# Optimization experiments

Measured on AMD Instinct MI355X. Metric: run time of the kernel, lower is better.

Reference implementation:

```python
import jax, jax.numpy as jnp
import numpy as np

N, D_IN, D_LAT, D_FEAT, K = 12000, 64, 16, 64, 16


def setup_inputs() -> dict:
    key = jax.random.key(0)
    ks = jax.random.split(key, 7)
    s_in = 1.0 / np.sqrt(D_IN)
    s_cat = 1.0 / np.sqrt(2 * D_FEAT)
    return {
        "x": jax.random.normal(ks[0], (N, D_IN), dtype=jnp.float32),
        "W_feat": jax.random.uniform(ks[1], (D_IN, D_FEAT), jnp.float32, -s_in, s_in),
        "b_feat": jax.random.uniform(ks[2], (D_FEAT,), jnp.float32, -s_in, s_in),
        "W_lat": jax.random.uniform(ks[3], (D_IN, D_LAT), jnp.float32, -s_in, s_in),
        "b_lat": jax.random.uniform(ks[4], (D_LAT,), jnp.float32, -s_in, s_in),
        "W_out": jax.random.uniform(ks[5], (2 * D_FEAT, D_FEAT), jnp.float32, -s_cat, s_cat),
        "b_out": jax.random.uniform(ks[6], (D_FEAT,), jnp.float32, -s_cat, s_cat),
    }


def reference(x, W_feat, b_feat, W_lat, b_lat, W_out, b_out):
    # dense encoders
    feats = jnp.tanh(x @ W_feat + b_feat)      # [N, F] learned features
    coords = jnp.tanh(x @ W_lat + b_lat)       # [N, S] latent coordinates
    n = coords.shape[0]
    # full pairwise squared euclidean distances (as the module's cdist)
    sq = jnp.sum(coords * coords, axis=1)
    d2 = sq[:, None] + sq[None, :] - 2.0 * (coords @ coords.T)   # [N, N]
    d2 = jnp.maximum(d2, 0.0)
    # knn_graph: k nearest neighbors, excluding self (loop=False)
    d2_masked = jnp.where(jnp.eye(n, dtype=bool), jnp.inf, d2)
    neg_d2, idx = jax.lax.top_k(-d2_masked, K)                   # idx: [N, K] neighbor (source) ids
    edge_d2 = -neg_d2                                            # squared dist to each neighbor
    # gaussian kernel on euclidean distance: w = exp(-d^2)
    w = jnp.exp(-edge_d2)                                        # [N, K]
    # message = w * x_j, aggr='add': out_i = sum_k w_ik * feats[idx_ik]
    agg = jnp.einsum('nk,nkf->nf', w, feats[idx])                # [N, F]
    # cat self features with aggregated messages, final dense
    out = jnp.concatenate([feats, agg], axis=1) @ W_out + b_out  # [N, F]
    return out
```

## Files before the change

kernel.cpp:

```cpp
#include <hip/hip_runtime.h>
#include <math.h>

typedef unsigned long long u64;
typedef _Float16 f16x8 __attribute__((ext_vector_type(8)));
typedef float f32x16 __attribute__((ext_vector_type(16)));

#define N_PTS 12000
#define KNN 16
#define QB 16
#define NWAVES 8
#define NGROUPS32 (N_PTS / 32)
#define TAU_PTS 2048
#define TAU_GROUPS32 (TAU_PTS / 32)
#define CAP 384
#define MARGIN 0.08f
#define EVICT_KEY ((u64)0x7F400000u << 32)

__global__ __launch_bounds__(256) void encoder_kernel(
    const float* __restrict__ x, const float* __restrict__ Wf, const float* __restrict__ bf,
    const float* __restrict__ Wl, const float* __restrict__ bl,
    float* __restrict__ feats, float* __restrict__ coords, _Float16* __restrict__ coords_h,
    float* __restrict__ sq)
{
  const int wave = threadIdx.x >> 6;
  const int lane = threadIdx.x & 63;
  const int i = blockIdx.x * 4 + wave;
  if (i >= N_PTS) return;
  float xv = x[i * 64 + lane];
  float accf = bf[lane];
  float accc = bl[lane & 15];
  #pragma unroll
  for (int k = 0; k < 64; ++k) {
    float xk = __shfl(xv, k);
    accf = fmaf(xk, Wf[k * 64 + lane], accf);
    accc = fmaf(xk, Wl[k * 16 + (lane & 15)], accc);
  }
  feats[i * 64 + lane] = tanhf(accf);
  float c = tanhf(accc);
  float cc = (lane < 16) ? c * c : 0.0f;
  cc += __shfl_xor(cc, 1);
  cc += __shfl_xor(cc, 2);
  cc += __shfl_xor(cc, 4);
  cc += __shfl_xor(cc, 8);
  if (lane < 16) {
    coords[i * 16 + lane] = c;
    coords_h[i * 16 + lane] = (_Float16)c;
  }
  if (lane == 0) sq[i] = cc;
}

__device__ __forceinline__ void ins6(u64 key, u64* k6, u64& kmax) {
  const u64 om = (key < kmax) ? kmax : ~0ull;
  #pragma unroll
  for (int t = 0; t < 6; ++t)
    k6[t] = (k6[t] == om) ? key : k6[t];
  u64 a = k6[0] > k6[1] ? k6[0] : k6[1];
  u64 b = k6[2] > k6[3] ? k6[2] : k6[3];
  u64 c = k6[4] > k6[5] ? k6[4] : k6[5];
  a = a > b ? a : b;
  kmax = a > c ? a : c;
}

__device__ __forceinline__ void ins8(u64 key, u64* k8, u64& kmax) {
  const u64 om = (key < kmax) ? kmax : ~0ull;
  #pragma unroll
  for (int t = 0; t < 8; ++t)
    k8[t] = (k8[t] == om) ? key : k8[t];
  u64 a = k8[0] > k8[1] ? k8[0] : k8[1];
  u64 b = k8[2] > k8[3] ? k8[2] : k8[3];
  u64 c = k8[4] > k8[5] ? k8[4] : k8[5];
  u64 d = k8[6] > k8[7] ? k8[6] : k8[7];
  a = a > b ? a : b;
  c = c > d ? c : d;
  kmax = a > c ? a : c;
}

__device__ __forceinline__ u64 shflx_u64(u64 v, int off) {
  int lo = __shfl_xor((int)(unsigned)v, off);
  int hi = __shfl_xor((int)(unsigned)(v >> 32), off);
  return ((u64)(unsigned)hi << 32) | (unsigned)lo;
}

__device__ __forceinline__ u64 minbfly(u64 m) {
  #pragma unroll
  for (int off = 32; off >= 1; off >>= 1) {
    u64 o = shflx_u64(m, off);
    m = (o < m) ? o : m;
  }
  return m;
}

#define CAS6(i, j) { const u64 a_ = k6[i], b_ = k6[j]; const bool sw_ = a_ > b_; \
                     k6[i] = sw_ ? b_ : a_; k6[j] = sw_ ? a_ : b_; }

__global__ __launch_bounds__(512) void knn_agg_kernel(
    const float* __restrict__ coords, const _Float16* __restrict__ coords_h,
    const float* __restrict__ sq, const float* __restrict__ feats,
    const float* __restrict__ Wo, const float* __restrict__ bo,
    float* __restrict__ out, int* __restrict__ flags)
{
  __shared__ unsigned short sbuf[QB][CAP];
  __shared__ int scnt[QB];
  __shared__ unsigned colminS[QB][64];
  __shared__ float taugS[QB];
  __shared__ __align__(16) float featS[QB][64];
  __shared__ __align__(16) float aggS[QB][64];

  const int tid = threadIdx.x;
  const int lane = tid & 63;
  const int wave = tid >> 6;
  const int qbase = blockIdx.x * QB;
  const int mcol = lane & 31;
  const int half = lane >> 5;

  if (tid < QB) scnt[tid] = 0;
  #pragma unroll
  for (int t = tid; t < QB * 64; t += 512)
    ((unsigned*)colminS)[t] = 0x7F800000u;

  f16x8 afrag = {0, 0, 0, 0, 0, 0, 0, 0};
  if (mcol < QB) {
    const uint4 u = *(const uint4*)((const char*)coords_h + (qbase + mcol) * 32 + half * 16);
    afrag = __builtin_bit_cast(f16x8, u);
  }
  float sqi8[8], nhsqi8[8];
  #pragma unroll
  for (int blk = 0; blk < 2; ++blk) {
    const float4 v = *(const float4*)&sq[qbase + blk * 8 + 4 * half];
    sqi8[blk * 4 + 0] = v.x; sqi8[blk * 4 + 1] = v.y;
    sqi8[blk * 4 + 2] = v.z; sqi8[blk * 4 + 3] = v.w;
  }
  #pragma unroll
  for (int r = 0; r < 8; ++r) nhsqi8[r] = -0.5f * sqi8[r];

  f32x16 acc;
  #pragma unroll
  for (int t = 0; t < 16; ++t) acc[t] = 0.0f;

  __syncthreads();

  const int g_self = qbase >> 5;
  float lmax8[8] = {-INFINITY, -INFINITY, -INFINITY, -INFINITY,
                    -INFINITY, -INFINITY, -INFINITY, -INFINITY};
  for (int g = wave; g < TAU_GROUPS32; g += NWAVES) {
    const int j0 = g * 32;
    const uint4 u = *(const uint4*)((const char*)coords_h + (j0 + mcol) * 32 + half * 16);
    const f16x8 bfrag = __builtin_bit_cast(f16x8, u);
    const float sqj = sq[j0 + mcol];
    #pragma unroll
    for (int r = 0; r < 8; ++r) acc[r] = fmaf(-0.5f, sqj, nhsqi8[r]);
    acc = __builtin_amdgcn_mfma_f32_32x32x16_f16(afrag, bfrag, acc, 0, 0, 0);
    if (g == g_self) {
      #pragma unroll
      for (int r = 0; r < 8; ++r) {
        const int row = (r >> 2) * 8 + 4 * half + (r & 3);
        if (j0 + mcol == qbase + row) acc[r] = -INFINITY;
      }
    }
    #pragma unroll
    for (int r = 0; r < 8; ++r) lmax8[r] = fmaxf(lmax8[r], acc[r]);
  }
  {
    const int cell = mcol * 2 + (wave >> 2);
    #pragma unroll
    for (int r = 0; r < 8; ++r) {
      const int row = (r >> 2) * 8 + 4 * half + (r & 3);
      atomicMin(&colminS[row][cell], __float_as_uint(fmaxf(-2.0f * lmax8[r], 0.0f)));
    }
  }
  __syncthreads();

  #pragma unroll
  for (int s = 0; s < 2; ++s) {
    const int q = wave * 2 + s;
    float v = __uint_as_float(colminS[q][lane]);
    #pragma unroll
    for (int k = 2; k <= 64; k <<= 1) {
      #pragma unroll
      for (int st = k >> 1; st >= 1; st >>= 1) {
        const float o = __shfl_xor(v, st);
        const bool keepMin = (((lane & st) == 0) == ((lane & k) == 0));
        const float mn = fminf(v, o), mx = fmaxf(v, o);
        v = keepMin ? mn : mx;
      }
    }
    const float tq = __shfl(v, 15) + MARGIN;
    if (lane == 0) taugS[q] = tq;
  }
  __syncthreads();

  float nht8[8];
  #pragma unroll
  for (int r = 0; r < 8; ++r)
    nht8[r] = -0.5f * taugS[(r >> 2) * 8 + 4 * half + (r & 3)];

  #pragma unroll 2
  for (int g = wave; g < NGROUPS32; g += NWAVES) {
    const int j0 = g * 32;
    const uint4 u = *(const uint4*)((const char*)coords_h + (j0 + mcol) * 32 + half * 16);
    const f16x8 bfrag = __builtin_bit_cast(f16x8, u);
    const float sqj = sq[j0 + mcol];
    #pragma unroll
    for (int r = 0; r < 8; ++r) acc[r] = fmaf(-0.5f, sqj, nhsqi8[r]);
    acc = __builtin_amdgcn_mfma_f32_32x32x16_f16(afrag, bfrag, acc, 0, 0, 0);
    #pragma unroll
    for (int r = 0; r < 8; ++r) {
      const bool pass = acc[r] >= nht8[r];
      if (__any(pass)) {
        if (pass) {
          const int row = (r >> 2) * 8 + 4 * half + (r & 3);
          const int p = atomicAdd(&scnt[row], 1);
          if (p < CAP) sbuf[row][p] = (unsigned short)(j0 + mcol);
        }
      }
    }
  }
  __syncthreads();

  #pragma unroll
  for (int s = 0; s < 2; ++s) {
    const int lq = wave * 2 + s;
    const int qg = qbase + lq;
    const int cq = scnt[lq];
    const int nread = (cq < CAP) ? cq : CAP;
    const int nit = (nread + 63) >> 6;

    float ci[16];
    {
      const float4* cp = (const float4*)(coords + qg * 16);
      *(float4*)&ci[0] = cp[0]; *(float4*)&ci[4] = cp[1];
      *(float4*)&ci[8] = cp[2]; *(float4*)&ci[12] = cp[3];
    }
    const float sqiq = sq[qg];

    u64 k6[6];
    #pragma unroll
    for (int t = 0; t < 6; ++t) k6[t] = ((u64)(0x7F000000u + t) << 32);
    u64 kmax6 = ((u64)0x7F000005u << 32);

    for (int t = 0; t < nit; ++t) {
      const int idx = t * 64 + lane;
      u64 key = ~0ull;
      if (idx < nread) {
        const int jj = sbuf[lq][idx];
        if (jj != qg) {
          const float4* cp = (const float4*)(coords + jj * 16);
          float cj[16];
          *(float4*)&cj[0]  = cp[0]; *(float4*)&cj[4]  = cp[1];
          *(float4*)&cj[8]  = cp[2]; *(float4*)&cj[12] = cp[3];
          float dot = 0.0f;
          #pragma unroll
          for (int d = 0; d < 16; ++d) dot = fmaf(ci[d], cj[d], dot);
          const float d2 = fmaxf(fmaf(-2.0f, dot, sqiq + sq[jj]), 0.0f);
          key = ((u64)__float_as_uint(d2) << 32) | (unsigned)jj;
        }
      }
      ins6(key, k6, kmax6);
    }

    CAS6(0,5) CAS6(1,3) CAS6(2,4)
    CAS6(1,2) CAS6(3,4)
    CAS6(0,3) CAS6(2,5)
    CAS6(0,1) CAS6(2,3) CAS6(4,5)
    CAS6(1,2) CAS6(3,4)

    float dmin = __uint_as_float((unsigned)(k6[0] >> 32));
    int jmin = (int)(unsigned)(k6[0] & 0xFFFFFFFFull);

    float dv[16]; int jv[16];
    #pragma unroll
    for (int r = 0; r < KNN; ++r) {
      float m = dmin;
      #pragma unroll
      for (int off = 32; off >= 1; off >>= 1)
        m = fminf(m, __shfl_xor(m, off));
      const u64 bal = __ballot(dmin == m);
      const int owner = __ffsll((unsigned long long)bal) - 1;
      jv[r] = __builtin_amdgcn_readlane(jmin, owner);
      dv[r] = __uint_as_float(__builtin_amdgcn_readfirstlane(__float_as_uint(m)));
      const bool me = (lane == owner);
      k6[0] = me ? k6[1] : k6[0];
      k6[1] = me ? k6[2] : k6[1];
      k6[2] = me ? k6[3] : k6[2];
      k6[3] = me ? k6[4] : k6[3];
      k6[4] = me ? k6[5] : k6[4];
      k6[5] = me ? EVICT_KEY : k6[5];
      dmin = __uint_as_float((unsigned)(k6[0] >> 32));
      jmin = (int)(unsigned)(k6[0] & 0xFFFFFFFFull);
    }

    float aggv = 0.0f;
    #pragma unroll
    for (int r = 0; r < KNN; ++r)
      aggv = fmaf(__expf(-dv[r]), feats[jv[r] * 64 + lane], aggv);

    aggS[lq][lane] = aggv;
    featS[lq][lane] = feats[qg * 64 + lane];
    if (lane == 0) flags[qg] = (cq > CAP);
  }

  __syncthreads();
  const int row = tid >> 5;
  const int c2 = (tid & 31) * 2;
  float acc0 = bo[c2], acc1 = bo[c2 + 1];
  #pragma unroll
  for (int f0 = 0; f0 < 64; f0 += 4) {
    const float4 fv = *(const float4*)&featS[row][f0];
    const float4 av = *(const float4*)&aggS[row][f0];
    #pragma unroll
    for (int u = 0; u < 4; ++u) {
      const float fvu = (u == 0) ? fv.x : (u == 1) ? fv.y : (u == 2) ? fv.z : fv.w;
      const float avu = (u == 0) ? av.x : (u == 1) ? av.y : (u == 2) ? av.z : av.w;
      const float2 w0 = *(const float2*)&Wo[(f0 + u) * 64 + c2];
      const float2 w1 = *(const float2*)&Wo[(64 + f0 + u) * 64 + c2];
      acc0 = fmaf(fvu, w0.x, acc0); acc0 = fmaf(avu, w1.x, acc0);
      acc1 = fmaf(fvu, w0.y, acc1); acc1 = fmaf(avu, w1.y, acc1);
    }
  }
  const int orow = qbase + row;
  *(float2*)&out[orow * 64 + c2] = make_float2(acc0, acc1);
}

__global__ __launch_bounds__(256) void knn_fixup_kernel(
    const float* __restrict__ coords, const float* __restrict__ sq,
    const float* __restrict__ feats, const int* __restrict__ flags,
    const float* __restrict__ Wo, const float* __restrict__ bo,
    float* __restrict__ out)
{
  const int wave = threadIdx.x >> 6;
  const int lane = threadIdx.x & 63;
  const int i = blockIdx.x * 4 + wave;
  if (i >= N_PTS) return;
  if (!flags[i]) return;
  float ci[16];
  #pragma unroll
  for (int d = 0; d < 16; ++d) ci[d] = coords[i * 16 + d];
  const float sqi = sq[i];

  u64 k8a[8], k8b[8], kmaxA, kmaxB;
  #pragma unroll
  for (int t = 0; t < 8; ++t) {
    k8a[t] = ((u64)(0x7F000000u + t) << 32);
    k8b[t] = ((u64)(0x7F000000u + t) << 32);
  }
  kmaxA = ((u64)0x7F000007u << 32);
  kmaxB = ((u64)0x7F000007u << 32);

  const int niter = (N_PTS + 63) / 64;
  for (int t = 0; t < niter; ++t) {
    const int j = t * 64 + lane;
    float4 c0 = make_float4(0,0,0,0), c1 = c0, c2 = c0, c3 = c0;
    float sqj = 0.0f;
    if (j < N_PTS) {
      const float4* cp = (const float4*)(coords + j * 16);
      c0 = cp[0]; c1 = cp[1]; c2 = cp[2]; c3 = cp[3];
      sqj = sq[j];
    }
    float dot = ci[0]*c0.x + ci[1]*c0.y + ci[2]*c0.z + ci[3]*c0.w
              + ci[4]*c1.x + ci[5]*c1.y + ci[6]*c1.z + ci[7]*c1.w
              + ci[8]*c2.x + ci[9]*c2.y + ci[10]*c2.z + ci[11]*c2.w
              + ci[12]*c3.x + ci[13]*c3.y + ci[14]*c3.z + ci[15]*c3.w;
    float d2 = fmaxf(fmaf(-2.0f, dot, sqi + sqj), 0.0f);
    const unsigned hi = (j == i || j >= N_PTS) ? 0xFFFFFFFFu : __float_as_uint(d2);
    const u64 key = ((u64)hi << 32) | (unsigned)j;
    if (t & 1) ins8(key, k8a, kmaxA);
    else       ins8(key, k8b, kmaxB);
  }

  u64 tab[16];
  #pragma unroll
  for (int t = 0; t < 8; ++t) { tab[t] = k8a[t]; tab[8 + t] = k8b[t]; }
  u64 lmin = tab[0];
  #pragma unroll
  for (int t = 1; t < 16; ++t) lmin = (tab[t] < lmin) ? tab[t] : lmin;

  float aggv = 0.0f;
  u64 T16 = 0;
  for (int r = 0; r < KNN; ++r) {
    const u64 m = minbfly(lmin);
    if (lmin == m) {
      #pragma unroll
      for (int t = 0; t < 16; ++t) tab[t] = (tab[t] == m) ? ~0ull : tab[t];
      lmin = tab[0];
      #pragma unroll
      for (int t = 1; t < 16; ++t) lmin = (tab[t] < lmin) ? tab[t] : lmin;
    }
    const unsigned hi = (unsigned)(m >> 32);
    const bool ok = hi < 0x7F000000u;
    const float w = ok ? expf(-__uint_as_float(hi)) : 0.0f;
    const int jj = ok ? (int)(unsigned)(m & 0xFFFFFFFFull) : 0;
    aggv = fmaf(w, feats[jj * 64 + lane], aggv);
    T16 = m;
  }

  if (__any((kmaxA < T16) || (kmaxB < T16))) {
    aggv = 0.0f;
    u64 prev = 0;
    for (int r = 0; r < KNN; ++r) {
      u64 best = ~0ull;
      for (int j = lane; j < N_PTS; j += 64) {
        float dot = 0.0f;
        #pragma unroll
        for (int d = 0; d < 16; ++d) dot = fmaf(ci[d], coords[j * 16 + d], dot);
        const float d2 = fmaxf(fmaf(-2.0f, dot, sqi + sq[j]), 0.0f);
        const unsigned hi = (j == i) ? 0xFFFFFFFFu : __float_as_uint(d2);
        const u64 key = ((u64)hi << 32) | (unsigned)j;
        const bool cand = (r == 0) || (key > prev);
        if (cand && key < best) best = key;
      }
      const u64 m = minbfly(best);
      prev = m;
      const unsigned hi = (unsigned)(m >> 32);
      const bool ok = hi < 0x7F000000u;
      const float w = ok ? expf(-__uint_as_float(hi)) : 0.0f;
      const int jj = ok ? (int)(unsigned)(m & 0xFFFFFFFFull) : 0;
      aggv = fmaf(w, feats[jj * 64 + lane], aggv);
    }
  }

  const float fl = feats[i * 64 + lane];
  float acc = bo[lane];
  #pragma unroll
  for (int f = 0; f < 64; ++f) {
    acc = fmaf(__shfl(fl, f),   Wo[f * 64 + lane],        acc);
    acc = fmaf(__shfl(aggv, f), Wo[(64 + f) * 64 + lane], acc);
  }
  out[i * 64 + lane] = acc;
}

extern "C" void kernel_launch(void* const* d_in, const int* in_sizes, int n_in,
                              void* d_out, int out_size, void* d_ws, size_t ws_size,
                              hipStream_t stream) {
  const float* x  = (const float*)d_in[0];
  const float* Wf = (const float*)d_in[1];
  const float* bf = (const float*)d_in[2];
  const float* Wl = (const float*)d_in[3];
  const float* bl = (const float*)d_in[4];
  const float* Wo = (const float*)d_in[5];
  const float* bo = (const float*)d_in[6];
  float* out = (float*)d_out;

  char* ws = (char*)d_ws;
  float*     feats    = (float*)(ws);
  float*     coords   = (float*)(ws + 3072000);
  float*     sqv      = (float*)(ws + 3840000);
  _Float16*  coords_h = (_Float16*)(ws + 3888000);
  int*       flags    = (int*)(ws + 4272000);

  encoder_kernel<<<3000, 256, 0, stream>>>(x, Wf, bf, Wl, bl, feats, coords, coords_h, sqv);
  knn_agg_kernel<<<N_PTS / QB, 512, 0, stream>>>(coords, coords_h, sqv, feats, Wo, bo, out, flags);
  knn_fixup_kernel<<<3000, 256, 0, stream>>>(coords, sqv, feats, flags, Wo, bo, out);
}
```

Baseline: 174.3 us.

## Prefetch coordinate tiles, split top-k merge across half-waves, double tau sample

Adds a three-deep register prefetch of coordinate fragments and squared norms in both the threshold-estimation and candidate-filtering MFMA loops, and removes the wave-wide any() guard. It also doubles the sample used to estimate the per-query distance threshold, splits the encoder's dot products into two accumulators, and sets occupancy launch bounds. The final 16-way selection now merges both queries' candidate lists at once, each half-wave working over 32 lanes and writing keys to shared memory. These aim to hide global load latency and shorten the serial selection, at the cost of more registers and twice the threshold-sampling work.

```diff
diff --git a/kernel.cpp b/kernel.cpp
--- a/kernel.cpp
+++ b/kernel.cpp
@@ -10,7 +10,7 @@
 #define QB 16
 #define NWAVES 8
 #define NGROUPS32 (N_PTS / 32)
-#define TAU_PTS 2048
+#define TAU_PTS 4096
 #define TAU_GROUPS32 (TAU_PTS / 32)
 #define CAP 384
 #define MARGIN 0.08f
@@ -27,16 +27,19 @@
   const int i = blockIdx.x * 4 + wave;
   if (i >= N_PTS) return;
   float xv = x[i * 64 + lane];
-  float accf = bf[lane];
-  float accc = bl[lane & 15];
-  #pragma unroll
-  for (int k = 0; k < 64; ++k) {
-    float xk = __shfl(xv, k);
-    accf = fmaf(xk, Wf[k * 64 + lane], accf);
-    accc = fmaf(xk, Wl[k * 16 + (lane & 15)], accc);
-  }
-  feats[i * 64 + lane] = tanhf(accf);
-  float c = tanhf(accc);
+  float accf0 = bf[lane], accf1 = 0.0f;
+  float accc0 = bl[lane & 15], accc1 = 0.0f;
+  #pragma unroll
+  for (int k = 0; k < 64; k += 2) {
+    const float xk0 = __shfl(xv, k);
+    const float xk1 = __shfl(xv, k + 1);
+    accf0 = fmaf(xk0, Wf[k * 64 + lane], accf0);
+    accf1 = fmaf(xk1, Wf[(k + 1) * 64 + lane], accf1);
+    accc0 = fmaf(xk0, Wl[k * 16 + (lane & 15)], accc0);
+    accc1 = fmaf(xk1, Wl[(k + 1) * 16 + (lane & 15)], accc1);
+  }
+  feats[i * 64 + lane] = tanhf(accf0 + accf1);
+  float c = tanhf(accc0 + accc1);
   float cc = (lane < 16) ? c * c : 0.0f;
   cc += __shfl_xor(cc, 1);
   cc += __shfl_xor(cc, 2);
@@ -93,7 +96,11 @@
 #define CAS6(i, j) { const u64 a_ = k6[i], b_ = k6[j]; const bool sw_ = a_ > b_; \
                      k6[i] = sw_ ? b_ : a_; k6[j] = sw_ ? a_ : b_; }
 
-__global__ __launch_bounds__(512) void knn_agg_kernel(
+#define LOADG(g, uu, ss) { const int jl_ = (g) * 32 + mcol; \
+  uu = *(const uint4*)((const char*)coords_h + (size_t)jl_ * 32 + half * 16); \
+  ss = sq[jl_]; }
+
+__global__ __launch_bounds__(512, 6) void knn_agg_kernel(
     const float* __restrict__ coords, const _Float16* __restrict__ coords_h,
     const float* __restrict__ sq, const float* __restrict__ feats,
     const float* __restrict__ Wo, const float* __restrict__ bo,
@@ -103,6 +110,7 @@
   __shared__ int scnt[QB];
   __shared__ unsigned colminS[QB][64];
   __shared__ float taugS[QB];
+  __shared__ u64 keyS[QB][KNN];
   __shared__ __align__(16) float featS[QB][64];
   __shared__ __align__(16) float aggS[QB][64];
 
@@ -123,15 +131,13 @@
     const uint4 u = *(const uint4*)((const char*)coords_h + (qbase + mcol) * 32 + half * 16);
     afrag = __builtin_bit_cast(f16x8, u);
   }
-  float sqi8[8], nhsqi8[8];
+  float nhsqi8[8];
   #pragma unroll
   for (int blk = 0; blk < 2; ++blk) {
     const float4 v = *(const float4*)&sq[qbase + blk * 8 + 4 * half];
-    sqi8[blk * 4 + 0] = v.x; sqi8[blk * 4 + 1] = v.y;
-    sqi8[blk * 4 + 2] = v.z; sqi8[blk * 4 + 3] = v.w;
-  }
-  #pragma unroll
-  for (int r = 0; r < 8; ++r) nhsqi8[r] = -0.5f * sqi8[r];
+    nhsqi8[blk * 4 + 0] = -0.5f * v.x; nhsqi8[blk * 4 + 1] = -0.5f * v.y;
+    nhsqi8[blk * 4 + 2] = -0.5f * v.z; nhsqi8[blk * 4 + 3] = -0.5f * v.w;
+  }
 
   f32x16 acc;
   #pragma unroll
@@ -142,23 +148,33 @@
   const int g_self = qbase >> 5;
   float lmax8[8] = {-INFINITY, -INFINITY, -INFINITY, -INFINITY,
                     -INFINITY, -INFINITY, -INFINITY, -INFINITY};
-  for (int g = wave; g < TAU_GROUPS32; g += NWAVES) {
-    const int j0 = g * 32;
-    const uint4 u = *(const uint4*)((const char*)coords_h + (j0 + mcol) * 32 + half * 16);
-    const f16x8 bfrag = __builtin_bit_cast(f16x8, u);
-    const float sqj = sq[j0 + mcol];
-    #pragma unroll
-    for (int r = 0; r < 8; ++r) acc[r] = fmaf(-0.5f, sqj, nhsqi8[r]);
-    acc = __builtin_amdgcn_mfma_f32_32x32x16_f16(afrag, bfrag, acc, 0, 0, 0);
-    if (g == g_self) {
-      #pragma unroll
-      for (int r = 0; r < 8; ++r) {
-        const int row = (r >> 2) * 8 + 4 * half + (r & 3);
-        if (j0 + mcol == qbase + row) acc[r] = -INFINITY;
+  {
+    uint4 pu0, pu1, pu2; float ps0, ps1, ps2;
+    LOADG(wave,                pu0, ps0);
+    LOADG(wave + NWAVES,       pu1, ps1);
+    LOADG(wave + 2 * NWAVES,   pu2, ps2);
+    for (int k = 0; k < 16; ++k) {
+      const int g = wave + k * NWAVES;
+      const uint4 cu = pu0; const float cs = ps0;
+      pu0 = pu1; ps0 = ps1; pu1 = pu2; ps1 = ps2;
+      const int kn = k + 3;
+      const int gs = (kn < 16) ? (wave + kn * NWAVES) : wave;
+      LOADG(gs, pu2, ps2);
+
+      const f16x8 bfrag = __builtin_bit_cast(f16x8, cu);
+      #pragma unroll
+      for (int r = 0; r < 8; ++r) acc[r] = fmaf(-0.5f, cs, nhsqi8[r]);
+      acc = __builtin_amdgcn_mfma_f32_32x32x16_f16(afrag, bfrag, acc, 0, 0, 0);
+      if (g == g_self) {
+        #pragma unroll
+        for (int r = 0; r < 8; ++r) {
+          const int row = (r >> 2) * 8 + 4 * half + (r & 3);
+          if (g * 32 + mcol == qbase + row) acc[r] = -INFINITY;
+        }
       }
-    }
-    #pragma unroll
-    for (int r = 0; r < 8; ++r) lmax8[r] = fmaxf(lmax8[r], acc[r]);
+      #pragma unroll
+      for (int r = 0; r < 8; ++r) lmax8[r] = fmaxf(lmax8[r], acc[r]);
+    }
   }
   {
     const int cell = mcol * 2 + (wave >> 2);
@@ -194,20 +210,26 @@
   for (int r = 0; r < 8; ++r)
     nht8[r] = -0.5f * taugS[(r >> 2) * 8 + 4 * half + (r & 3)];
 
-  #pragma unroll 2
-  for (int g = wave; g < NGROUPS32; g += NWAVES) {
-    const int j0 = g * 32;
-    const uint4 u = *(const uint4*)((const char*)coords_h + (j0 + mcol) * 32 + half * 16);
-    const f16x8 bfrag = __builtin_bit_cast(f16x8, u);
-    const float sqj = sq[j0 + mcol];
-    #pragma unroll
-    for (int r = 0; r < 8; ++r) acc[r] = fmaf(-0.5f, sqj, nhsqi8[r]);
-    acc = __builtin_amdgcn_mfma_f32_32x32x16_f16(afrag, bfrag, acc, 0, 0, 0);
-    #pragma unroll
-    for (int r = 0; r < 8; ++r) {
-      const bool pass = acc[r] >= nht8[r];
-      if (__any(pass)) {
-        if (pass) {
+  {
+    uint4 pu0, pu1, pu2; float ps0, ps1, ps2;
+    LOADG(wave,                pu0, ps0);
+    LOADG(wave + NWAVES,       pu1, ps1);
+    LOADG(wave + 2 * NWAVES,   pu2, ps2);
+    for (int g = wave; g < NGROUPS32; g += NWAVES) {
+      const uint4 cu = pu0; const float cs = ps0;
+      pu0 = pu1; ps0 = ps1; pu1 = pu2; ps1 = ps2;
+      const int gn = g + 3 * NWAVES;
+      const int gs = (gn < NGROUPS32) ? gn : wave;
+      LOADG(gs, pu2, ps2);
+
+      const f16x8 bfrag = __builtin_bit_cast(f16x8, cu);
+      #pragma unroll
+      for (int r = 0; r < 8; ++r) acc[r] = fmaf(-0.5f, cs, nhsqi8[r]);
+      acc = __builtin_amdgcn_mfma_f32_32x32x16_f16(afrag, bfrag, acc, 0, 0, 0);
+      const int j0 = g * 32;
+      #pragma unroll
+      for (int r = 0; r < 8; ++r) {
+        if (acc[r] >= nht8[r]) {
           const int row = (r >> 2) * 8 + 4 * half + (r & 3);
           const int p = atomicAdd(&scnt[row], 1);
           if (p < CAP) sbuf[row][p] = (unsigned short)(j0 + mcol);
@@ -216,6 +238,9 @@
     }
   }
   __syncthreads();
+
+  const int h = lane >> 5;
+  u64 Al[6], Bl[6];
 
   #pragma unroll
   for (int s = 0; s < 2; ++s) {
@@ -245,12 +270,21 @@
         const int jj = sbuf[lq][idx];
         if (jj != qg) {
           const float4* cp = (const float4*)(coords + jj * 16);
-          float cj[16];
-          *(float4*)&cj[0]  = cp[0]; *(float4*)&cj[4]  = cp[1];
-          *(float4*)&cj[8]  = cp[2]; *(float4*)&cj[12] = cp[3];
           float dot = 0.0f;
-          #pragma unroll
-          for (int d = 0; d < 16; ++d) dot = fmaf(ci[d], cj[d], dot);
+          {
+            const float4 c0 = cp[0], c1 = cp[1];
+            dot = fmaf(ci[0], c0.x, dot); dot = fmaf(ci[1], c0.y, dot);
+            dot = fmaf(ci[2], c0.z, dot); dot = fmaf(ci[3], c0.w, dot);
+            dot = fmaf(ci[4], c1.x, dot); dot = fmaf(ci[5], c1.y, dot);
+            dot = fmaf(ci[6], c1.z, dot); dot = fmaf(ci[7], c1.w, dot);
+          }
+          {
+            const float4 c2 = cp[2], c3 = cp[3];
+            dot = fmaf(ci[8],  c2.x, dot); dot = fmaf(ci[9],  c2.y, dot);
+            dot = fmaf(ci[10], c2.z, dot); dot = fmaf(ci[11], c2.w, dot);
+            dot = fmaf(ci[12], c3.x, dot); dot = fmaf(ci[13], c3.y, dot);
+            dot = fmaf(ci[14], c3.z, dot); dot = fmaf(ci[15], c3.w, dot);
+          }
           const float d2 = fmaxf(fmaf(-2.0f, dot, sqiq + sq[jj]), 0.0f);
           key = ((u64)__float_as_uint(d2) << 32) | (unsigned)jj;
         }
@@ -264,39 +298,52 @@
     CAS6(0,1) CAS6(2,3) CAS6(4,5)
     CAS6(1,2) CAS6(3,4)
 
-    float dmin = __uint_as_float((unsigned)(k6[0] >> 32));
-    int jmin = (int)(unsigned)(k6[0] & 0xFFFFFFFFull);
-
-    float dv[16]; int jv[16];
+    #pragma unroll
+    for (int t = 0; t < 6; ++t) {
+      const u64 p = shflx_u64(k6[t], 32);
+      if (h == s) { Al[t] = k6[t]; Bl[t] = p; }
+    }
+    if (lane == 0) flags[qg] = (cq > CAP);
+  }
+
+  {
+    u64 myhead = (Al[0] < Bl[0]) ? Al[0] : Bl[0];
     #pragma unroll
     for (int r = 0; r < KNN; ++r) {
-      float m = dmin;
-      #pragma unroll
-      for (int off = 32; off >= 1; off >>= 1)
-        m = fminf(m, __shfl_xor(m, off));
-      const u64 bal = __ballot(dmin == m);
-      const int owner = __ffsll((unsigned long long)bal) - 1;
-      jv[r] = __builtin_amdgcn_readlane(jmin, owner);
-      dv[r] = __uint_as_float(__builtin_amdgcn_readfirstlane(__float_as_uint(m)));
-      const bool me = (lane == owner);
-      k6[0] = me ? k6[1] : k6[0];
-      k6[1] = me ? k6[2] : k6[1];
-      k6[2] = me ? k6[3] : k6[2];
-      k6[3] = me ? k6[4] : k6[3];
-      k6[4] = me ? k6[5] : k6[4];
-      k6[5] = me ? EVICT_KEY : k6[5];
-      dmin = __uint_as_float((unsigned)(k6[0] >> 32));
-      jmin = (int)(unsigned)(k6[0] & 0xFFFFFFFFull);
-    }
-
+      u64 m = myhead;
+      #pragma unroll
+      for (int off = 16; off >= 1; off >>= 1) {
+        const u64 o = shflx_u64(m, off);
+        m = (o < m) ? o : m;
+      }
+      if ((lane & 31) == 0) keyS[wave * 2 + h][r] = m;
+      const bool me = (myhead == m);
+      const bool fa = me && (Al[0] == m);
+      const bool fb = me && !fa;
+      Al[0] = fa ? Al[1] : Al[0]; Al[1] = fa ? Al[2] : Al[1];
+      Al[2] = fa ? Al[3] : Al[2]; Al[3] = fa ? Al[4] : Al[3];
+      Al[4] = fa ? Al[5] : Al[4]; Al[5] = fa ? EVICT_KEY : Al[5];
+      Bl[0] = fb ? Bl[1] : Bl[0]; Bl[1] = fb ? Bl[2] : Bl[1];
+      Bl[2] = fb ? Bl[3] : Bl[2]; Bl[3] = fb ? Bl[4] : Bl[3];
+      Bl[4] = fb ? Bl[5] : Bl[4]; Bl[5] = fb ? EVICT_KEY : Bl[5];
+      myhead = (Al[0] < Bl[0]) ? Al[0] : Bl[0];
+    }
+  }
+
+  #pragma unroll
+  for (int s = 0; s < 2; ++s) {
+    const int lq = wave * 2 + s;
+    const int qg = qbase + lq;
     float aggv = 0.0f;
     #pragma unroll
-    for (int r = 0; r < KNN; ++r)
-      aggv = fmaf(__expf(-dv[r]), feats[jv[r] * 64 + lane], aggv);
-
+    for (int r = 0; r < KNN; ++r) {
+      const u64 m = keyS[lq][r];
+      const float w = __expf(-__uint_as_float((unsigned)(m >> 32)));
+      const int jj = (int)(unsigned)(m & 0xFFFFFFFFull);
+      aggv = fmaf(w, feats[jj * 64 + lane], aggv);
+    }
     aggS[lq][lane] = aggv;
     featS[lq][lane] = feats[qg * 64 + lane];
-    if (lane == 0) flags[qg] = (cq > CAP);
   }
 
   __syncthreads();
```

Measured after the change: 172.2 us. About the same (-1.3%).
